# Performance work log

Measured on AMD Instinct MI355X. Metric: run time of the kernel, lower is better.

The kernel has to match this reference:

```python
import jax, jax.numpy as jnp
import numpy as np

B, T, E, D = 8, 2048, 1024, 64  # batch, seq, embed_dim, head_dim

def setup_inputs() -> dict:
    key = jax.random.key(0)
    kx, kq, kk, kv = jax.random.split(key, 4)
    scale = 1.0 / np.sqrt(E)
    return {
        "x": jax.random.normal(kx, (B, T, E), dtype=jnp.float32),
        "Wq": jax.random.normal(kq, (E, D), dtype=jnp.float32) * scale,
        "Wk": jax.random.normal(kk, (E, D), dtype=jnp.float32) * scale,
        "Wv": jax.random.normal(kv, (E, D), dtype=jnp.float32) * scale,
    }

def reference(x, Wq, Wk, Wv):
    # single-head causal attention (dropout in eval mode = identity)
    q = jnp.einsum('bte,ed->btd', x, Wq)
    k = jnp.einsum('bte,ed->btd', x, Wk)
    v = jnp.einsum('bte,ed->btd', x, Wv)
    head_dim = q.shape[-1]
    wei = jnp.einsum('btd,bsd->bts', q, k) * (head_dim ** -0.5)  # [B,T,T]
    causal = jnp.tril(jnp.ones((wei.shape[1], wei.shape[2]), dtype=bool))
    wei = jnp.where(causal, wei, -jnp.inf)
    wei = jax.nn.softmax(wei, axis=-1)
    out = jnp.einsum('bts,bsd->btd', wei, v)  # [B,T,D]
    return out
```

## Files before the change

kernel.cpp:

```cpp
#include <hip/hip_runtime.h>
#include <hip/hip_bf16.h>
#include <cstdint>
#include <cstddef>

#define B_ 8
#define T_ 2048
#define E_ 1024
#define D_ 64

typedef __attribute__((ext_vector_type(8))) short bf16x8;
typedef __attribute__((ext_vector_type(4))) float f32x4;
typedef __attribute__((ext_vector_type(16))) float f32x16;
typedef __attribute__((ext_vector_type(4))) unsigned short u16x4;

#define QSCALE 0.1803368801111204f

__device__ __forceinline__ short f2bf(float f){
    __hip_bfloat16 h = __float2bfloat16(f);
    return *reinterpret_cast<short*>(&h);
}

__device__ __forceinline__ bf16x8 cvt8v(const f32x4 a, const f32x4 b){
    bf16x8 r;
    r[0]=f2bf(a[0]); r[1]=f2bf(a[1]); r[2]=f2bf(a[2]); r[3]=f2bf(a[3]);
    r[4]=f2bf(b[0]); r[5]=f2bf(b[1]); r[6]=f2bf(b[2]); r[7]=f2bf(b[3]);
    return r;
}

__global__ __launch_bounds__(256) void wconv_kernel(
    const float* __restrict__ Wq, const float* __restrict__ Wk,
    const float* __restrict__ Wv, __hip_bfloat16* __restrict__ Wfrag)
{
    const int g = blockIdx.x*256 + threadIdx.x;
    const int l = g & 63;
    const int ntg = (g >> 6) % 6;
    const int cg = g / 384;
    const int n = ntg*32 + (l & 31);
    const int m = n >> 6;
    const int ncol = n & 63;
    const float* W = (m==0) ? Wq : (m==1) ? Wk : Wv;
    const float sc = (m==0) ? QSCALE : 1.0f;
    const int k0 = cg*16 + (l>>5)*8;
    bf16x8 r;
    #pragma unroll
    for (int j=0;j<8;++j)
        r[j] = f2bf(W[(size_t)(k0+j)*64 + ncol] * sc);
    *reinterpret_cast<bf16x8*>(Wfrag + (size_t)g*8) = r;
}

__global__ __launch_bounds__(384, 3) void proj_kernel(
    const float* __restrict__ x, const __hip_bfloat16* __restrict__ Wfrag,
    __hip_bfloat16* __restrict__ Qfrag, __hip_bfloat16* __restrict__ Kfrag,
    __hip_bfloat16* __restrict__ Vfrag)
{
    __shared__ __align__(16) unsigned short xs[2][32*64];
    __shared__ float vtQ[32*65];
    __shared__ float vtK[32*65];
    __shared__ float vtV[32*65];
    const int tid = threadIdx.x;
    const int w = tid>>6, l = tid&63;
    const int l31 = l&31, kg = l>>5;
    const float* xp = x + (size_t)blockIdx.x*32*E_;

    f32x16 acc;
    #pragma unroll
    for (int j=0;j<16;++j) acc[j]=0.f;

    const bf16x8* Wfp = reinterpret_cast<const bf16x8*>(Wfrag);

    bf16x8 btA[4], btB[4];
    #pragma unroll
    for (int c=0;c<4;++c)
        btA[c] = Wfp[(size_t)(((0*4+c)*6 + w)*64 + l)];

    const int srow = tid>>3, sc8 = tid&7;

    if (tid < 256){
        f32x4 v0 = *reinterpret_cast<const f32x4*>(xp + (size_t)srow*E_ + sc8*8);
        f32x4 v1 = *reinterpret_cast<const f32x4*>(xp + (size_t)srow*E_ + sc8*8 + 4);
        *reinterpret_cast<bf16x8*>((char*)&xs[0][0] + srow*128 + ((sc8*16) ^ ((srow&7)<<4))) = cvt8v(v0, v1);
    }
    __syncthreads();

#define PSTEP(T, BC, BN)                                                       \
    {                                                                          \
        const int t = (T);                                                     \
        if (t+1 < 16){                                                         \
            _Pragma("unroll")                                                  \
            for (int c=0;c<4;++c)                                              \
                BN[c] = Wfp[(size_t)((((t+1)*4+c)*6 + w)*64 + l)];             \
        }                                                                      \
        f32x4 xa0, xa1;                                                        \
        if (t+1 < 16 && tid < 256){                                            \
            xa0 = *reinterpret_cast<const f32x4*>(xp + (size_t)srow*E_ + (t+1)*64 + sc8*8);     \
            xa1 = *reinterpret_cast<const f32x4*>(xp + (size_t)srow*E_ + (t+1)*64 + sc8*8 + 4); \
        }                                                                      \
        const char* xb = (const char*)&xs[t&1][0];                             \
        _Pragma("unroll")                                                      \
        for (int c=0;c<4;++c){                                                 \
            bf16x8 af = *reinterpret_cast<const bf16x8*>(xb + l31*128 + (((c*32 + kg*16)) ^ ((l31&7)<<4))); \
            acc = __builtin_amdgcn_mfma_f32_32x32x16_bf16(af, BC[c], acc, 0,0,0); \
        }                                                                      \
        if (t+1 < 16){                                                         \
            if (tid < 256)                                                     \
                *reinterpret_cast<bf16x8*>((char*)&xs[(t+1)&1][0] + srow*128 + ((sc8*16) ^ ((srow&7)<<4))) = cvt8v(xa0, xa1); \
            __syncthreads();                                                   \
        }                                                                      \
    }

    for (int t2=0; t2<8; ++t2){
        PSTEP(2*t2,   btA, btB)
        PSTEP(2*t2+1, btB, btA)
    }
#undef PSTEP

    {
        float* vtX = (w<2) ? vtQ : (w<4) ? vtK : vtV;
        const int col = (w&1)*32 + l31;
        #pragma unroll
        for (int reg=0; reg<16; ++reg){
            const int mr = (reg&3) + 8*(reg>>2) + 4*kg;
            vtX[mr*65 + col] = acc[reg];
        }
    }
    __syncthreads();
    if (tid < 256){
        const int q = blockIdx.x, b = q>>6, q63 = q&63, t = q63>>1;
        const int su  = (tid>>7)&1, ksw = (tid>>6)&1, lw = tid&63;
        const int lw15 = lw&15, lwg = lw>>4;
        {
            f32x4 a0, a1;
            #pragma unroll
            for (int j=0;j<4;++j) a0[j] = vtQ[(su*16+lw15)*65 + ksw*32 + lwg*8 + j];
            #pragma unroll
            for (int j=0;j<4;++j) a1[j] = vtQ[(su*16+lw15)*65 + ksw*32 + lwg*8 + 4 + j];
            const size_t gi = ((size_t)(b*128 + 2*q63 + su)*2 + ksw)*64 + lw;
            *reinterpret_cast<bf16x8*>(Qfrag + gi*8) = cvt8v(a0, a1);
        }
        {
            f32x4 a0, a1;
            #pragma unroll
            for (int j=0;j<4;++j) a0[j] = vtK[(su*16+lw15)*65 + ksw*32 + lwg*8 + j];
            #pragma unroll
            for (int j=0;j<4;++j) a1[j] = vtK[(su*16+lw15)*65 + ksw*32 + lwg*8 + 4 + j];
            const int nt = (q&1)*2 + su;
            const size_t gi = (((size_t)(b*32 + t)*4 + nt)*2 + ksw)*64 + lw;
            *reinterpret_cast<bf16x8*>(Kfrag + gi*8) = cvt8v(a0, a1);
        }
        {
            const int dt = tid>>6;
            bf16x8 pk;
            #pragma unroll
            for (int j=0;j<8;++j)
                pk[j] = f2bf(vtV[(lwg*8+j)*65 + dt*16 + lw15]);
            const size_t gi = (((size_t)(b*32 + t)*4 + dt)*2 + (q&1))*64 + lw;
            *reinterpret_cast<bf16x8*>(Vfrag + gi*8) = pk;
        }
    }
}

__global__ __launch_bounds__(256, 2) void fattn_kernel(
    const __hip_bfloat16* __restrict__ Qfrag, const __hip_bfloat16* __restrict__ Kfrag,
    const __hip_bfloat16* __restrict__ Vfrag, float* __restrict__ out)
{
    __shared__ __align__(16) unsigned short Pl[4][16*64];
    __shared__ float Morg[4][2][16];
    __shared__ float Lorg[4][2][16];
    __shared__ __align__(16) float Oorg[4][2][16*64];

    const int tid = threadIdx.x;
    const int w = tid>>6, l = tid&63;
    const int l15 = l&15, lg = l>>4;

    const int b = blockIdx.x & 7;
    const int p = blockIdx.x >> 3;
    const int sA = p, sB = 127 - p;
    const int nA = (sA>>2) + 1, nB = (sB>>2) + 1;
    const int NU = nA + nB;
    const size_t batchoff = (size_t)b * T_ * 64;

    const bf16x8* qfp = reinterpret_cast<const bf16x8*>(Qfrag);
    const bf16x8* kfp = reinterpret_cast<const bf16x8*>(Kfrag);
    const bf16x8* vfp = reinterpret_cast<const bf16x8*>(Vfrag);
    char* pw = (char*)&Pl[w][0];

    const int qrA = sA*16 + l15, qrB = sB*16 + l15;
    const bf16x8 qA0 = qfp[(size_t)((b*128 + sA)*2 + 0)*64 + l];
    const bf16x8 qA1 = qfp[(size_t)((b*128 + sA)*2 + 1)*64 + l];
    const bf16x8 qB0 = qfp[(size_t)((b*128 + sB)*2 + 0)*64 + l];
    const bf16x8 qB1 = qfp[(size_t)((b*128 + sB)*2 + 1)*64 + l];

    f32x4 oA[4], oB[4];
    #pragma unroll
    for (int i=0;i<4;++i){ oA[i] = (f32x4){0.f,0.f,0.f,0.f}; oB[i] = (f32x4){0.f,0.f,0.f,0.f}; }
    float mA = -1e30f, lA = 0.f, mB = -1e30f, lB = 0.f;

    bf16x8 kf[8], vf[8];

    {
        const int u0 = w;
        const int kvt = (u0 < nA ? u0 : u0 - nA);
        #pragma unroll
        for (int ks=0;ks<2;++ks)
            #pragma unroll
            for (int nt=0;nt<4;++nt)
                kf[ks*4+nt] = kfp[(size_t)(((b*32 + kvt)*4 + nt)*2 + ks)*64 + l];
    }

    auto body = [&](f32x4 (&o)[4], float &mrun, float &lrun,
                    const bf16x8 &qf0, const bf16x8 &qf1,
                    int qrow, int kv0, bool diag, bool hasN, int kvtn)
    {
        f32x4 s4[4];
        #pragma unroll
        for (int nt=0;nt<4;++nt) s4[nt] = (f32x4){0.f,0.f,0.f,0.f};
        __builtin_amdgcn_s_setprio(1);
        #pragma unroll
        for (int ks=0;ks<2;++ks){
            const bf16x8 qf = ks ? qf1 : qf0;
            #pragma unroll
            for (int nt=0;nt<4;++nt)
                s4[nt] = __builtin_amdgcn_mfma_f32_16x16x32_bf16(kf[ks*4+nt], qf, s4[nt], 0,0,0);
        }
        __builtin_amdgcn_s_setprio(0);

        if (hasN){
            #pragma unroll
            for (int ks=0;ks<2;++ks)
                #pragma unroll
                for (int nt=0;nt<4;++nt)
                    kf[ks*4+nt] = kfp[(size_t)(((b*32 + kvtn)*4 + nt)*2 + ks)*64 + l];
        }

        if (diag){
            #pragma unroll
            for (int nt=0;nt<4;++nt)
                #pragma unroll
                for (int rr=0;rr<4;++rr){
                    const int kv = kv0 + nt*16 + lg*4 + rr;
                    if (kv > qrow) s4[nt][rr] = -1e30f;
                }
        }

        float pm;
        {
            float m0 = fmaxf(fmaxf(s4[0][0],s4[0][1]), fmaxf(s4[0][2],s4[0][3]));
            float m1 = fmaxf(fmaxf(s4[1][0],s4[1][1]), fmaxf(s4[1][2],s4[1][3]));
            float m2 = fmaxf(fmaxf(s4[2][0],s4[2][1]), fmaxf(s4[2][2],s4[2][3]));
            float m3 = fmaxf(fmaxf(s4[3][0],s4[3][1]), fmaxf(s4[3][2],s4[3][3]));
            pm = fmaxf(fmaxf(m0,m1), fmaxf(m2,m3));
        }
        pm = fmaxf(pm, __shfl_xor(pm, 16));
        pm = fmaxf(pm, __shfl_xor(pm, 32));
        if (pm > mrun + 8.0f){
            const float scl = exp2f(mrun - pm);
            mrun = pm; lrun *= scl;
            #pragma unroll
            for (int dt=0;dt<4;++dt)
                #pragma unroll
                for (int j=0;j<4;++j) o[dt][j] *= scl;
        }
        float rs = 0.f;
        #pragma unroll
        for (int nt=0;nt<4;++nt)
            #pragma unroll
            for (int rr=0;rr<4;++rr){
                const float pv = exp2f(s4[nt][rr] - mrun);
                s4[nt][rr] = pv; rs += pv;
            }
        rs += __shfl_xor(rs, 16);
        rs += __shfl_xor(rs, 32);
        lrun += rs;

        #pragma unroll
        for (int nt=0;nt<4;++nt){
            u16x4 pk;
            #pragma unroll
            for (int rr=0;rr<4;++rr) pk[rr] = (unsigned short)f2bf(s4[nt][rr]);
            *reinterpret_cast<u16x4*>(pw + l15*128 + ((nt*32 + lg*8) ^ ((l15&7)<<4))) = pk;
        }

        __builtin_amdgcn_s_setprio(1);
        #pragma unroll
        for (int ks=0;ks<2;++ks){
            bf16x8 pf = *reinterpret_cast<const bf16x8*>(pw + l15*128 + ((ks*64 + lg*16) ^ ((l15&7)<<4)));
            #pragma unroll
            for (int dt=0;dt<4;++dt)
                o[dt] = __builtin_amdgcn_mfma_f32_16x16x32_bf16(vf[ks*4+dt], pf, o[dt], 0,0,0);
        }
        __builtin_amdgcn_s_setprio(0);
    };

    for (int u = w; u < NU; u += 4){
        const bool isA = (u < nA);
        const int kvt = isA ? u : (u - nA);
        const int kv0 = kvt*64;
        const bool diag = isA ? (kvt == nA-1) : (kvt == nB-1);

        #pragma unroll
        for (int ks=0;ks<2;++ks)
            #pragma unroll
            for (int dt=0;dt<4;++dt)
                vf[ks*4+dt] = vfp[(size_t)(((b*32 + kvt)*4 + dt)*2 + ks)*64 + l];

        const int un = u + 4;
        const bool hasN = un < NU;
        const int kvtn = hasN ? (un < nA ? un : un - nA) : 0;

        if (isA) body(oA, mA, lA, qA0, qA1, qrA, kv0, diag, hasN, kvtn);
        else     body(oB, mB, lB, qB0, qB1, qrB, kv0, diag, hasN, kvtn);
    }

    #pragma unroll
    for (int dt=0;dt<4;++dt){
        *reinterpret_cast<f32x4*>(&Oorg[w][0][l15*64 + dt*16 + lg*4]) = oA[dt];
        *reinterpret_cast<f32x4*>(&Oorg[w][1][l15*64 + dt*16 + lg*4]) = oB[dt];
    }
    if (lg == 0){
        Morg[w][0][l15] = mA; Lorg[w][0][l15] = lA;
        Morg[w][1][l15] = mB; Lorg[w][1][l15] = lB;
    }
    __syncthreads();
    {
        const int h = tid>>7, q = (tid>>3)&15, d0 = (tid&7)*8;
        const float m0=Morg[0][h][q], m1=Morg[1][h][q], m2=Morg[2][h][q], m3=Morg[3][h][q];
        const float M = fmaxf(fmaxf(m0,m1), fmaxf(m2,m3));
        const float a0=exp2f(m0-M), a1=exp2f(m1-M), a2=exp2f(m2-M), a3=exp2f(m3-M);
        const float L = a0*Lorg[0][h][q] + a1*Lorg[1][h][q] + a2*Lorg[2][h][q] + a3*Lorg[3][h][q];
        const float inv = 1.0f / L;
        const int s = h ? sB : sA;
        float* op = out + batchoff + (size_t)(s*16 + q)*64 + d0;
        #pragma unroll
        for (int j=0;j<8;++j){
            const float v = a0*Oorg[0][h][q*64+d0+j] + a1*Oorg[1][h][q*64+d0+j]
                          + a2*Oorg[2][h][q*64+d0+j] + a3*Oorg[3][h][q*64+d0+j];
            op[j] = v * inv;
        }
    }
}

extern "C" void kernel_launch(void* const* d_in, const int* in_sizes, int n_in,
                              void* d_out, int out_size, void* d_ws, size_t ws_size,
                              hipStream_t stream) {
    const float* x  = (const float*)d_in[0];
    const float* Wq = (const float*)d_in[1];
    const float* Wk = (const float*)d_in[2];
    const float* Wv = (const float*)d_in[3];
    float* out = (float*)d_out;

    const size_t NTOK = (size_t)B_*T_*64;
    __hip_bfloat16* Wfrag = (__hip_bfloat16*)d_ws;
    __hip_bfloat16* Qfrag = Wfrag + (size_t)24576*8;
    __hip_bfloat16* Kfrag = Qfrag + NTOK;
    __hip_bfloat16* Vfrag = Kfrag + NTOK;

    wconv_kernel<<<96, 256, 0, stream>>>(Wq, Wk, Wv, Wfrag);
    proj_kernel<<<512, 384, 0, stream>>>(x, Wfrag, Qfrag, Kfrag, Vfrag);
    fattn_kernel<<<512, 256, 0, stream>>>(Qfrag, Kfrag, Vfrag, out);
}
```

Measured before the change: 41.27 us.

## Process KV tiles in pairs per wave and defer row-sum reduction

Restructures the per-wave KV loop so each wave handles two KV tiles at once, issuing both K and V loads up front and interleaving two independent MFMA chains for better latency hiding. The software prefetch of the next K tile is replaced by bulk loads inside each pair. The row-sum cross-lane shuffles are removed; per-lane partial sums are stored and reduced in the final merge. The max-rescale shuffles run only when some lane exceeds the threshold. This raises register pressure and doubles the P staging buffer in shared memory.

```diff
diff --git a/kernel.cpp b/kernel.cpp
--- a/kernel.cpp
+++ b/kernel.cpp
@@ -163,9 +163,9 @@
     const __hip_bfloat16* __restrict__ Qfrag, const __hip_bfloat16* __restrict__ Kfrag,
     const __hip_bfloat16* __restrict__ Vfrag, float* __restrict__ out)
 {
-    __shared__ __align__(16) unsigned short Pl[4][16*64];
+    __shared__ __align__(16) unsigned short Pl[4][2048];
     __shared__ float Morg[4][2][16];
-    __shared__ float Lorg[4][2][16];
+    __shared__ float Lorg[4][2][64];
     __shared__ __align__(16) float Oorg[4][2][16*64];
 
     const int tid = threadIdx.x;
@@ -176,7 +176,6 @@
     const int p = blockIdx.x >> 3;
     const int sA = p, sB = 127 - p;
     const int nA = (sA>>2) + 1, nB = (sB>>2) + 1;
-    const int NU = nA + nB;
     const size_t batchoff = (size_t)b * T_ * 64;
 
     const bf16x8* qfp = reinterpret_cast<const bf16x8*>(Qfrag);
@@ -195,22 +194,18 @@
     for (int i=0;i<4;++i){ oA[i] = (f32x4){0.f,0.f,0.f,0.f}; oB[i] = (f32x4){0.f,0.f,0.f,0.f}; }
     float mA = -1e30f, lA = 0.f, mB = -1e30f, lB = 0.f;
 
-    bf16x8 kf[8], vf[8];
-
+    auto single = [&](f32x4 (&o)[4], float &mrun, float &lrun,
+                      const bf16x8 &qf0, const bf16x8 &qf1,
+                      int qrow, int kvt, int n)
     {
-        const int u0 = w;
-        const int kvt = (u0 < nA ? u0 : u0 - nA);
+        bf16x8 kf[8], vf[8];
         #pragma unroll
         for (int ks=0;ks<2;++ks)
             #pragma unroll
-            for (int nt=0;nt<4;++nt)
+            for (int nt=0;nt<4;++nt){
                 kf[ks*4+nt] = kfp[(size_t)(((b*32 + kvt)*4 + nt)*2 + ks)*64 + l];
-    }
-
-    auto body = [&](f32x4 (&o)[4], float &mrun, float &lrun,
-                    const bf16x8 &qf0, const bf16x8 &qf1,
-                    int qrow, int kv0, bool diag, bool hasN, int kvtn)
-    {
+                vf[ks*4+nt] = vfp[(size_t)(((b*32 + kvt)*4 + nt)*2 + ks)*64 + l];
+            }
         f32x4 s4[4];
         #pragma unroll
         for (int nt=0;nt<4;++nt) s4[nt] = (f32x4){0.f,0.f,0.f,0.f};
@@ -224,15 +219,8 @@
         }
         __builtin_amdgcn_s_setprio(0);
 
-        if (hasN){
-            #pragma unroll
-            for (int ks=0;ks<2;++ks)
-                #pragma unroll
-                for (int nt=0;nt<4;++nt)
-                    kf[ks*4+nt] = kfp[(size_t)(((b*32 + kvtn)*4 + nt)*2 + ks)*64 + l];
-        }
-
-        if (diag){
+        if (kvt == n-1){
+            const int kv0 = kvt*64;
             #pragma unroll
             for (int nt=0;nt<4;++nt)
                 #pragma unroll
@@ -242,19 +230,21 @@
                 }
         }
 
-        float pm;
+        float pmLoc;
         {
             float m0 = fmaxf(fmaxf(s4[0][0],s4[0][1]), fmaxf(s4[0][2],s4[0][3]));
             float m1 = fmaxf(fmaxf(s4[1][0],s4[1][1]), fmaxf(s4[1][2],s4[1][3]));
             float m2 = fmaxf(fmaxf(s4[2][0],s4[2][1]), fmaxf(s4[2][2],s4[2][3]));
             float m3 = fmaxf(fmaxf(s4[3][0],s4[3][1]), fmaxf(s4[3][2],s4[3][3]));
-            pm = fmaxf(fmaxf(m0,m1), fmaxf(m2,m3));
-        }
-        pm = fmaxf(pm, __shfl_xor(pm, 16));
-        pm = fmaxf(pm, __shfl_xor(pm, 32));
-        if (pm > mrun + 8.0f){
-            const float scl = exp2f(mrun - pm);
-            mrun = pm; lrun *= scl;
+            pmLoc = fmaxf(fmaxf(m0,m1), fmaxf(m2,m3));
+        }
+        if (__any(pmLoc > mrun + 8.0f)){
+            float pm = pmLoc;
+            pm = fmaxf(pm, __shfl_xor(pm, 16));
+            pm = fmaxf(pm, __shfl_xor(pm, 32));
+            const float mn = fmaxf(mrun, pm);
+            const float scl = exp2f(mrun - mn);
+            mrun = mn; lrun *= scl;
             #pragma unroll
             for (int dt=0;dt<4;++dt)
                 #pragma unroll
@@ -268,8 +258,6 @@
                 const float pv = exp2f(s4[nt][rr] - mrun);
                 s4[nt][rr] = pv; rs += pv;
             }
-        rs += __shfl_xor(rs, 16);
-        rs += __shfl_xor(rs, 32);
         lrun += rs;
 
         #pragma unroll
@@ -279,7 +267,6 @@
             for (int rr=0;rr<4;++rr) pk[rr] = (unsigned short)f2bf(s4[nt][rr]);
             *reinterpret_cast<u16x4*>(pw + l15*128 + ((nt*32 + lg*8) ^ ((l15&7)<<4))) = pk;
         }
-
         __builtin_amdgcn_s_setprio(1);
         #pragma unroll
         for (int ks=0;ks<2;++ks){
@@ -291,34 +278,139 @@
         __builtin_amdgcn_s_setprio(0);
     };
 
-    for (int u = w; u < NU; u += 4){
-        const bool isA = (u < nA);
-        const int kvt = isA ? u : (u - nA);
-        const int kv0 = kvt*64;
-        const bool diag = isA ? (kvt == nA-1) : (kvt == nB-1);
-
+    auto dual = [&](f32x4 (&o)[4], float &mrun, float &lrun,
+                    const bf16x8 &qf0, const bf16x8 &qf1,
+                    int qrow, int kvt1, int kvt2, int n)
+    {
+        bf16x8 kf1[8], kf2[8], vf1[8], vf2[8];
         #pragma unroll
         for (int ks=0;ks<2;++ks)
             #pragma unroll
+            for (int nt=0;nt<4;++nt){
+                kf1[ks*4+nt] = kfp[(size_t)(((b*32 + kvt1)*4 + nt)*2 + ks)*64 + l];
+                kf2[ks*4+nt] = kfp[(size_t)(((b*32 + kvt2)*4 + nt)*2 + ks)*64 + l];
+            }
+        #pragma unroll
+        for (int ks=0;ks<2;++ks)
+            #pragma unroll
+            for (int nt=0;nt<4;++nt){
+                vf1[ks*4+nt] = vfp[(size_t)(((b*32 + kvt1)*4 + nt)*2 + ks)*64 + l];
+                vf2[ks*4+nt] = vfp[(size_t)(((b*32 + kvt2)*4 + nt)*2 + ks)*64 + l];
+            }
+
+        f32x4 s41[4], s42[4];
+        #pragma unroll
+        for (int nt=0;nt<4;++nt){ s41[nt] = (f32x4){0.f,0.f,0.f,0.f}; s42[nt] = (f32x4){0.f,0.f,0.f,0.f}; }
+        __builtin_amdgcn_s_setprio(1);
+        #pragma unroll
+        for (int ks=0;ks<2;++ks){
+            const bf16x8 qf = ks ? qf1 : qf0;
+            #pragma unroll
+            for (int nt=0;nt<4;++nt)
+                s41[nt] = __builtin_amdgcn_mfma_f32_16x16x32_bf16(kf1[ks*4+nt], qf, s41[nt], 0,0,0);
+            #pragma unroll
+            for (int nt=0;nt<4;++nt)
+                s42[nt] = __builtin_amdgcn_mfma_f32_16x16x32_bf16(kf2[ks*4+nt], qf, s42[nt], 0,0,0);
+        }
+        __builtin_amdgcn_s_setprio(0);
+
+        if (kvt2 == n-1){
+            const int kv0 = kvt2*64;
+            #pragma unroll
+            for (int nt=0;nt<4;++nt)
+                #pragma unroll
+                for (int rr=0;rr<4;++rr){
+                    const int kv = kv0 + nt*16 + lg*4 + rr;
+                    if (kv > qrow) s42[nt][rr] = -1e30f;
+                }
+        }
+
+        float pmLoc;
+        {
+            float a0 = fmaxf(fmaxf(s41[0][0],s41[0][1]), fmaxf(s41[0][2],s41[0][3]));
+            float a1 = fmaxf(fmaxf(s41[1][0],s41[1][1]), fmaxf(s41[1][2],s41[1][3]));
+            float a2 = fmaxf(fmaxf(s41[2][0],s41[2][1]), fmaxf(s41[2][2],s41[2][3]));
+            float a3 = fmaxf(fmaxf(s41[3][0],s41[3][1]), fmaxf(s41[3][2],s41[3][3]));
+            float b0 = fmaxf(fmaxf(s42[0][0],s42[0][1]), fmaxf(s42[0][2],s42[0][3]));
+            float b1 = fmaxf(fmaxf(s42[1][0],s42[1][1]), fmaxf(s42[1][2],s42[1][3]));
+            float b2 = fmaxf(fmaxf(s42[2][0],s42[2][1]), fmaxf(s42[2][2],s42[2][3]));
+            float b3 = fmaxf(fmaxf(s42[3][0],s42[3][1]), fmaxf(s42[3][2],s42[3][3]));
+            pmLoc = fmaxf(fmaxf(fmaxf(a0,a1), fmaxf(a2,a3)),
+                          fmaxf(fmaxf(b0,b1), fmaxf(b2,b3)));
+        }
+        if (__any(pmLoc > mrun + 8.0f)){
+            float pm = pmLoc;
+            pm = fmaxf(pm, __shfl_xor(pm, 16));
+            pm = fmaxf(pm, __shfl_xor(pm, 32));
+            const float mn = fmaxf(mrun, pm);
+            const float scl = exp2f(mrun - mn);
+            mrun = mn; lrun *= scl;
+            #pragma unroll
             for (int dt=0;dt<4;++dt)
-                vf[ks*4+dt] = vfp[(size_t)(((b*32 + kvt)*4 + dt)*2 + ks)*64 + l];
-
-        const int un = u + 4;
-        const bool hasN = un < NU;
-        const int kvtn = hasN ? (un < nA ? un : un - nA) : 0;
-
-        if (isA) body(oA, mA, lA, qA0, qA1, qrA, kv0, diag, hasN, kvtn);
-        else     body(oB, mB, lB, qB0, qB1, qrB, kv0, diag, hasN, kvtn);
-    }
+                #pragma unroll
+                for (int j=0;j<4;++j) o[dt][j] *= scl;
+        }
+        float rs = 0.f;
+        #pragma unroll
+        for (int nt=0;nt<4;++nt)
+            #pragma unroll
+            for (int rr=0;rr<4;++rr){
+                const float pv1 = exp2f(s41[nt][rr] - mrun);
+                const float pv2 = exp2f(s42[nt][rr] - mrun);
+                s41[nt][rr] = pv1; s42[nt][rr] = pv2;
+                rs += pv1 + pv2;
+            }
+        lrun += rs;
+
+        #pragma unroll
+        for (int nt=0;nt<4;++nt){
+            u16x4 pk1, pk2;
+            #pragma unroll
+            for (int rr=0;rr<4;++rr){
+                pk1[rr] = (unsigned short)f2bf(s41[nt][rr]);
+                pk2[rr] = (unsigned short)f2bf(s42[nt][rr]);
+            }
+            *reinterpret_cast<u16x4*>(pw + l15*128 + ((nt*32 + lg*8) ^ ((l15&7)<<4))) = pk1;
+            *reinterpret_cast<u16x4*>(pw + 2048 + l15*128 + ((nt*32 + lg*8) ^ ((l15&7)<<4))) = pk2;
+        }
+        __builtin_amdgcn_s_setprio(1);
+        #pragma unroll
+        for (int ks=0;ks<2;++ks){
+            bf16x8 pf1 = *reinterpret_cast<const bf16x8*>(pw + l15*128 + ((ks*64 + lg*16) ^ ((l15&7)<<4)));
+            bf16x8 pf2 = *reinterpret_cast<const bf16x8*>(pw + 2048 + l15*128 + ((ks*64 + lg*16) ^ ((l15&7)<<4)));
+            #pragma unroll
+            for (int dt=0;dt<4;++dt)
+                o[dt] = __builtin_amdgcn_mfma_f32_16x16x32_bf16(vf1[ks*4+dt], pf1, o[dt], 0,0,0);
+            #pragma unroll
+            for (int dt=0;dt<4;++dt)
+                o[dt] = __builtin_amdgcn_mfma_f32_16x16x32_bf16(vf2[ks*4+dt], pf2, o[dt], 0,0,0);
+        }
+        __builtin_amdgcn_s_setprio(0);
+    };
+
+    const int tot  = (33 - w + 3) >> 2;
+    const int aCnt = (nA > w) ? ((nA - w + 3) >> 2) : 0;
+    const int bCnt = tot - aCnt;
+
+    for (int i=0; i+1 < aCnt; i += 2)
+        dual(oA, mA, lA, qA0, qA1, qrA, w + 4*i, w + 4*(i+1), nA);
+    if (aCnt & 1)
+        single(oA, mA, lA, qA0, qA1, qrA, w + 4*(aCnt-1), nA);
+    for (int j=0; j+1 < bCnt; j += 2)
+        dual(oB, mB, lB, qB0, qB1, qrB, w + 4*(aCnt+j) - nA, w + 4*(aCnt+j+1) - nA, nB);
+    if (bCnt & 1)
+        single(oB, mB, lB, qB0, qB1, qrB, w + 4*(aCnt+bCnt-1) - nA, nB);
 
     #pragma unroll
     for (int dt=0;dt<4;++dt){
         *reinterpret_cast<f32x4*>(&Oorg[w][0][l15*64 + dt*16 + lg*4]) = oA[dt];
         *reinterpret_cast<f32x4*>(&Oorg[w][1][l15*64 + dt*16 + lg*4]) = oB[dt];
     }
+    Lorg[w][0][l] = lA;
+    Lorg[w][1][l] = lB;
     if (lg == 0){
-        Morg[w][0][l15] = mA; Lorg[w][0][l15] = lA;
-        Morg[w][1][l15] = mB; Lorg[w][1][l15] = lB;
+        Morg[w][0][l15] = mA;
+        Morg[w][1][l15] = mB;
     }
     __syncthreads();
     {
@@ -326,7 +418,12 @@
         const float m0=Morg[0][h][q], m1=Morg[1][h][q], m2=Morg[2][h][q], m3=Morg[3][h][q];
         const float M = fmaxf(fmaxf(m0,m1), fmaxf(m2,m3));
         const float a0=exp2f(m0-M), a1=exp2f(m1-M), a2=exp2f(m2-M), a3=exp2f(m3-M);
-        const float L = a0*Lorg[0][h][q] + a1*Lorg[1][h][q] + a2*Lorg[2][h][q] + a3*Lorg[3][h][q];
+        float L = 0.f;
+        #pragma unroll
+        for (int gg=0; gg<4; ++gg){
+            L += a0*Lorg[0][h][gg*16+q] + a1*Lorg[1][h][gg*16+q]
+               + a2*Lorg[2][h][gg*16+q] + a3*Lorg[3][h][gg*16+q];
+        }
         const float inv = 1.0f / L;
         const int s = h ? sB : sA;
         float* op = out + batchoff + (size_t)(s*16 + q)*64 + d0;
```

Measured after the change: 39.81 us. 1.04x faster.

## Split paired query tiles into separate blocks with heavy-first ordering

Applied to the files above, without the earlier changes.

The attention kernel now gives each block a single 16-row query tile instead of a balanced pair, doubling the grid to 1024 blocks. Tiles are scheduled longest first, and the occupancy hint rises to 4 blocks per CU. The next-K-tile register prefetch is dropped in favour of loading K and V at the start of each iteration. The per-tile row-sum shuffles move into the final merge, and the max rescale is skipped using a wave-level any-vote. The aim is more parallelism and fewer registers per wave, at the cost of less latency hiding per wave and a finer-grained load imbalance.

```diff
diff --git a/kernel.cpp b/kernel.cpp
--- a/kernel.cpp
+++ b/kernel.cpp
@@ -159,24 +159,24 @@
     }
 }
 
-__global__ __launch_bounds__(256, 2) void fattn_kernel(
+__global__ __launch_bounds__(256, 4) void fattn_kernel(
     const __hip_bfloat16* __restrict__ Qfrag, const __hip_bfloat16* __restrict__ Kfrag,
     const __hip_bfloat16* __restrict__ Vfrag, float* __restrict__ out)
 {
-    __shared__ __align__(16) unsigned short Pl[4][16*64];
-    __shared__ float Morg[4][2][16];
-    __shared__ float Lorg[4][2][16];
-    __shared__ __align__(16) float Oorg[4][2][16*64];
+    __shared__ __align__(16) unsigned short Pl[4][1024];
+    __shared__ float Morg[4][16];
+    __shared__ float Lorg[4][64];
+    __shared__ __align__(16) float Oorg[4][16*64];
 
     const int tid = threadIdx.x;
     const int w = tid>>6, l = tid&63;
     const int l15 = l&15, lg = l>>4;
 
     const int b = blockIdx.x & 7;
-    const int p = blockIdx.x >> 3;
-    const int sA = p, sB = 127 - p;
-    const int nA = (sA>>2) + 1, nB = (sB>>2) + 1;
-    const int NU = nA + nB;
+    const int g = blockIdx.x >> 8;
+    const int r = (blockIdx.x >> 3) & 31;
+    const int s = (g==0) ? (127 - r) : (g==1) ? (64 + r) : (g==2) ? (63 - r) : r;
+    const int n = (s>>2) + 1;
     const size_t batchoff = (size_t)b * T_ * 64;
 
     const bf16x8* qfp = reinterpret_cast<const bf16x8*>(Qfrag);
@@ -184,33 +184,24 @@
     const bf16x8* vfp = reinterpret_cast<const bf16x8*>(Vfrag);
     char* pw = (char*)&Pl[w][0];
 
-    const int qrA = sA*16 + l15, qrB = sB*16 + l15;
-    const bf16x8 qA0 = qfp[(size_t)((b*128 + sA)*2 + 0)*64 + l];
-    const bf16x8 qA1 = qfp[(size_t)((b*128 + sA)*2 + 1)*64 + l];
-    const bf16x8 qB0 = qfp[(size_t)((b*128 + sB)*2 + 0)*64 + l];
-    const bf16x8 qB1 = qfp[(size_t)((b*128 + sB)*2 + 1)*64 + l];
-
-    f32x4 oA[4], oB[4];
-    #pragma unroll
-    for (int i=0;i<4;++i){ oA[i] = (f32x4){0.f,0.f,0.f,0.f}; oB[i] = (f32x4){0.f,0.f,0.f,0.f}; }
-    float mA = -1e30f, lA = 0.f, mB = -1e30f, lB = 0.f;
-
-    bf16x8 kf[8], vf[8];
-
-    {
-        const int u0 = w;
-        const int kvt = (u0 < nA ? u0 : u0 - nA);
+    const int qrow = s*16 + l15;
+    const bf16x8 qf0 = qfp[(size_t)((b*128 + s)*2 + 0)*64 + l];
+    const bf16x8 qf1 = qfp[(size_t)((b*128 + s)*2 + 1)*64 + l];
+
+    f32x4 o[4];
+    #pragma unroll
+    for (int i=0;i<4;++i) o[i] = (f32x4){0.f,0.f,0.f,0.f};
+    float mrun = -1e30f, lrun = 0.f;
+
+    for (int kvt = w; kvt < n; kvt += 4){
+        bf16x8 kf[8], vf[8];
         #pragma unroll
         for (int ks=0;ks<2;++ks)
             #pragma unroll
-            for (int nt=0;nt<4;++nt)
+            for (int nt=0;nt<4;++nt){
                 kf[ks*4+nt] = kfp[(size_t)(((b*32 + kvt)*4 + nt)*2 + ks)*64 + l];
-    }
-
-    auto body = [&](f32x4 (&o)[4], float &mrun, float &lrun,
-                    const bf16x8 &qf0, const bf16x8 &qf1,
-                    int qrow, int kv0, bool diag, bool hasN, int kvtn)
-    {
+                vf[ks*4+nt] = vfp[(size_t)(((b*32 + kvt)*4 + nt)*2 + ks)*64 + l];
+            }
         f32x4 s4[4];
         #pragma unroll
         for (int nt=0;nt<4;++nt) s4[nt] = (f32x4){0.f,0.f,0.f,0.f};
@@ -224,15 +215,8 @@
         }
         __builtin_amdgcn_s_setprio(0);
 
-        if (hasN){
-            #pragma unroll
-            for (int ks=0;ks<2;++ks)
-                #pragma unroll
-                for (int nt=0;nt<4;++nt)
-                    kf[ks*4+nt] = kfp[(size_t)(((b*32 + kvtn)*4 + nt)*2 + ks)*64 + l];
-        }
-
-        if (diag){
+        if (kvt == n-1){
+            const int kv0 = kvt*64;
             #pragma unroll
             for (int nt=0;nt<4;++nt)
                 #pragma unroll
@@ -242,19 +226,21 @@
                 }
         }
 
-        float pm;
+        float pmLoc;
         {
             float m0 = fmaxf(fmaxf(s4[0][0],s4[0][1]), fmaxf(s4[0][2],s4[0][3]));
             float m1 = fmaxf(fmaxf(s4[1][0],s4[1][1]), fmaxf(s4[1][2],s4[1][3]));
             float m2 = fmaxf(fmaxf(s4[2][0],s4[2][1]), fmaxf(s4[2][2],s4[2][3]));
             float m3 = fmaxf(fmaxf(s4[3][0],s4[3][1]), fmaxf(s4[3][2],s4[3][3]));
-            pm = fmaxf(fmaxf(m0,m1), fmaxf(m2,m3));
-        }
-        pm = fmaxf(pm, __shfl_xor(pm, 16));
-        pm = fmaxf(pm, __shfl_xor(pm, 32));
-        if (pm > mrun + 8.0f){
-            const float scl = exp2f(mrun - pm);
-            mrun = pm; lrun *= scl;
+            pmLoc = fmaxf(fmaxf(m0,m1), fmaxf(m2,m3));
+        }
+        if (__any(pmLoc > mrun + 8.0f)){
+            float pm = pmLoc;
+            pm = fmaxf(pm, __shfl_xor(pm, 16));
+            pm = fmaxf(pm, __shfl_xor(pm, 32));
+            const float mn = fmaxf(mrun, pm);
+            const float scl = exp2f(mrun - mn);
+            mrun = mn; lrun *= scl;
             #pragma unroll
             for (int dt=0;dt<4;++dt)
                 #pragma unroll
@@ -268,8 +254,6 @@
                 const float pv = exp2f(s4[nt][rr] - mrun);
                 s4[nt][rr] = pv; rs += pv;
             }
-        rs += __shfl_xor(rs, 16);
-        rs += __shfl_xor(rs, 32);
         lrun += rs;
 
         #pragma unroll
@@ -279,7 +263,6 @@
             for (int rr=0;rr<4;++rr) pk[rr] = (unsigned short)f2bf(s4[nt][rr]);
             *reinterpret_cast<u16x4*>(pw + l15*128 + ((nt*32 + lg*8) ^ ((l15&7)<<4))) = pk;
         }
-
         __builtin_amdgcn_s_setprio(1);
         #pragma unroll
         for (int ks=0;ks<2;++ks){
@@ -289,51 +272,31 @@
                 o[dt] = __builtin_amdgcn_mfma_f32_16x16x32_bf16(vf[ks*4+dt], pf, o[dt], 0,0,0);
         }
         __builtin_amdgcn_s_setprio(0);
-    };
-
-    for (int u = w; u < NU; u += 4){
-        const bool isA = (u < nA);
-        const int kvt = isA ? u : (u - nA);
-        const int kv0 = kvt*64;
-        const bool diag = isA ? (kvt == nA-1) : (kvt == nB-1);
-
-        #pragma unroll
-        for (int ks=0;ks<2;++ks)
-            #pragma unroll
-            for (int dt=0;dt<4;++dt)
-                vf[ks*4+dt] = vfp[(size_t)(((b*32 + kvt)*4 + dt)*2 + ks)*64 + l];
-
-        const int un = u + 4;
-        const bool hasN = un < NU;
-        const int kvtn = hasN ? (un < nA ? un : un - nA) : 0;
-
-        if (isA) body(oA, mA, lA, qA0, qA1, qrA, kv0, diag, hasN, kvtn);
-        else     body(oB, mB, lB, qB0, qB1, qrB, kv0, diag, hasN, kvtn);
-    }
-
-    #pragma unroll
-    for (int dt=0;dt<4;++dt){
-        *reinterpret_cast<f32x4*>(&Oorg[w][0][l15*64 + dt*16 + lg*4]) = oA[dt];
-        *reinterpret_cast<f32x4*>(&Oorg[w][1][l15*64 + dt*16 + lg*4]) = oB[dt];
-    }
-    if (lg == 0){
-        Morg[w][0][l15] = mA; Lorg[w][0][l15] = lA;
-        Morg[w][1][l15] = mB; Lorg[w][1][l15] = lB;
-    }
+    }
+
+    #pragma unroll
+    for (int dt=0;dt<4;++dt)
+        *reinterpret_cast<f32x4*>(&Oorg[w][l15*64 + dt*16 + lg*4]) = o[dt];
+    Lorg[w][l] = lrun;
+    if (lg == 0) Morg[w][l15] = mrun;
     __syncthreads();
     {
-        const int h = tid>>7, q = (tid>>3)&15, d0 = (tid&7)*8;
-        const float m0=Morg[0][h][q], m1=Morg[1][h][q], m2=Morg[2][h][q], m3=Morg[3][h][q];
+        const int q = tid >> 4, dg = tid & 15;
+        const float m0=Morg[0][q], m1=Morg[1][q], m2=Morg[2][q], m3=Morg[3][q];
         const float M = fmaxf(fmaxf(m0,m1), fmaxf(m2,m3));
         const float a0=exp2f(m0-M), a1=exp2f(m1-M), a2=exp2f(m2-M), a3=exp2f(m3-M);
-        const float L = a0*Lorg[0][h][q] + a1*Lorg[1][h][q] + a2*Lorg[2][h][q] + a3*Lorg[3][h][q];
+        float L = 0.f;
+        #pragma unroll
+        for (int lgg=0; lgg<4; ++lgg){
+            L += a0*Lorg[0][lgg*16+q] + a1*Lorg[1][lgg*16+q]
+               + a2*Lorg[2][lgg*16+q] + a3*Lorg[3][lgg*16+q];
+        }
         const float inv = 1.0f / L;
-        const int s = h ? sB : sA;
-        float* op = out + batchoff + (size_t)(s*16 + q)*64 + d0;
-        #pragma unroll
-        for (int j=0;j<8;++j){
-            const float v = a0*Oorg[0][h][q*64+d0+j] + a1*Oorg[1][h][q*64+d0+j]
-                          + a2*Oorg[2][h][q*64+d0+j] + a3*Oorg[3][h][q*64+d0+j];
+        float* op = out + batchoff + (size_t)(s*16 + q)*64 + dg*4;
+        #pragma unroll
+        for (int j=0;j<4;++j){
+            const float v = a0*Oorg[0][q*64+dg*4+j] + a1*Oorg[1][q*64+dg*4+j]
+                          + a2*Oorg[2][q*64+dg*4+j] + a3*Oorg[3][q*64+dg*4+j];
             op[j] = v * inv;
         }
     }
@@ -356,5 +319,5 @@
 
     wconv_kernel<<<96, 256, 0, stream>>>(Wq, Wk, Wv, Wfrag);
     proj_kernel<<<512, 384, 0, stream>>>(x, Wfrag, Qfrag, Kfrag, Vfrag);
-    fattn_kernel<<<512, 256, 0, stream>>>(Qfrag, Kfrag, Vfrag, out);
-}
+    fattn_kernel<<<1024, 256, 0, stream>>>(Qfrag, Kfrag, Vfrag, out);
+}
```

Result: faster. 37.76 us (-8.5%).
